# Kernel tuning notes

Hardware: AMD Instinct MI355X
Metric: run time of the kernel (lower is better)

Reference implementation:

```python
import jax, jax.numpy as jnp
import numpy as np
from jax import lax

B, T, D = 4, 4096, 1024  # d_inner == D (expansion=1.0)


def setup_inputs() -> dict:
    key = jax.random.key(0)
    ks = jax.random.split(key, 6)
    s = 1.0 / np.sqrt(D)  # xavier-ish scale
    return {
        "x": jax.random.normal(ks[0], (B, T, D), dtype=jnp.float32),
        "W_in": jax.random.normal(ks[1], (D, D), dtype=jnp.float32) * s,
        "W_alpha": jax.random.normal(ks[2], (D, D), dtype=jnp.float32) * s,
        "b_alpha": jnp.full((D,), 2.0, dtype=jnp.float32),
        "W_beta": jax.random.normal(ks[3], (D, D), dtype=jnp.float32) * s,
        "b_beta": jnp.zeros((D,), dtype=jnp.float32),
        "W_v": jax.random.normal(ks[4], (D, D), dtype=jnp.float32) * s,
        "b_v": jnp.zeros((D,), dtype=jnp.float32),
        "W_out": jax.random.normal(ks[5], (D, D), dtype=jnp.float32) * s,
    }


def reference(x, W_in, W_alpha, b_alpha, W_beta, b_beta, W_v, b_v, W_out):
    # x: [B, T, D]; torch nn.Linear convention y = x @ W.T
    xp = jax.nn.silu(jnp.einsum("btd,ed->bte", x, W_in))  # [B, T, Di]
    alpha = jax.nn.sigmoid(jnp.einsum("bte,fe->btf", xp, W_alpha) + b_alpha)
    beta = jax.nn.sigmoid(jnp.einsum("bte,fe->btf", xp, W_beta) + b_beta)
    v = jnp.tanh(jnp.einsum("bte,fe->btf", xp, W_v) + b_v)
    bv = beta * v  # precompute write term

    def step(h, ab):
        a_t, bv_t = ab  # each [B, Di]
        h = a_t * h + bv_t
        return h, h * jax.nn.silu(h)

    h0 = jnp.zeros((x.shape[0], W_alpha.shape[0]), dtype=x.dtype)
    h_last, outs = lax.scan(step, h0, (alpha.transpose(1, 0, 2), bv.transpose(1, 0, 2)))
    cell_out = outs.transpose(1, 0, 2)  # [B, T, Di]
    output = jnp.einsum("btf,df->btd", cell_out, W_out)
    return output, h_last
```

## Files before the change

### kernel.cpp

```cpp
#include <hip/hip_runtime.h>
#include <hip/hip_bf16.h>
#include <cstdint>
#include <cstddef>

typedef __bf16 bf16_t;
typedef __bf16 bf16x8 __attribute__((ext_vector_type(8)));
typedef float  f32x4  __attribute__((ext_vector_type(4)));

constexpr int kBatch = 4;
constexpr int kT = 4096;
constexpr int kD = 1024;
constexpr int kM = kBatch * kT;
constexpr int kCH = kBatch * kD;
constexpr int kNC = 128;
constexpr int kL  = kT / kNC;
constexpr int LDS_BYTES = 131072;

__device__ __forceinline__ void async16(const bf16_t* g, char* l) {
    __builtin_amdgcn_global_load_lds(
        (const __attribute__((address_space(1))) uint32_t*)g,
        (__attribute__((address_space(3))) uint32_t*)l,
        16, 0, 0);
}

__global__ void cvt_bf16_kernel(const float* __restrict__ in, bf16_t* __restrict__ out, int n8) {
    int i = blockIdx.x * blockDim.x + threadIdx.x;
    if (i >= n8) return;
    const float4* p = reinterpret_cast<const float4*>(in) + 2 * (size_t)i;
    float4 a = p[0], b = p[1];
    bf16x8 o;
    o[0] = (bf16_t)a.x; o[1] = (bf16_t)a.y; o[2] = (bf16_t)a.z; o[3] = (bf16_t)a.w;
    o[4] = (bf16_t)b.x; o[5] = (bf16_t)b.y; o[6] = (bf16_t)b.z; o[7] = (bf16_t)b.w;
    *reinterpret_cast<bf16x8*>(out + 8 * (size_t)i) = o;
}

__global__ void cvtw_kernel(const float* __restrict__ w0, const float* __restrict__ w1,
                            const float* __restrict__ w2, const float* __restrict__ w3,
                            const float* __restrict__ w4, bf16_t* __restrict__ out) {
    const int per = kD * kD / 8;
    int i = blockIdx.x * blockDim.x + threadIdx.x;
    int seg = i / per, j = i - seg * per;
    const float* src = seg == 0 ? w0 : seg == 1 ? w1 : seg == 2 ? w2 : seg == 3 ? w3 : w4;
    const float4* p = reinterpret_cast<const float4*>(src) + 2 * (size_t)j;
    float4 a = p[0], b = p[1];
    bf16x8 o;
    o[0] = (bf16_t)a.x; o[1] = (bf16_t)a.y; o[2] = (bf16_t)a.z; o[3] = (bf16_t)a.w;
    o[4] = (bf16_t)b.x; o[5] = (bf16_t)b.y; o[6] = (bf16_t)b.z; o[7] = (bf16_t)b.w;
    *reinterpret_cast<bf16x8*>(out + ((size_t)seg * per + j) * 8) = o;
}

template<int EPI>
__global__ __launch_bounds__(512, 2)
void gemm256(const bf16_t* __restrict__ A, const bf16_t* __restrict__ Bw,
             const float* __restrict__ bi0, const float* __restrict__ bi1,
             const float* __restrict__ bi2,
             void* __restrict__ out0, void* __restrict__ out1, void* __restrict__ out2,
             int M, int N, int K)
{
    extern __shared__ char lds[];
    const int tid  = threadIdx.x;
    const int lane = tid & 63;
    const int wv   = tid >> 6;
    const int wr   = wv >> 2;
    const int wc   = wv & 3;
    const int l16  = lane & 15;
    const int lhi  = lane >> 4;

    int bid = blockIdx.y * gridDim.x + blockIdx.x;
    int nwg = gridDim.x * gridDim.y;
    int swz = (bid & 7) * (nwg >> 3) + (bid >> 3);
    int gx  = N >> 8;
    int n0  = (swz % gx) << 8;
    int m0  = (swz / gx) << 8;

    auto goff = [&](int chunk) -> size_t {
        int st = chunk >> 6;
        int ri = (chunk >> 2) & 15;
        int cp = (chunk & 3) << 3;
        int cl = cp ^ (((ri >> 3) & 1) << 4);
        int gr = ((st >> 1) << 4) + ri;
        int gc = ((st & 1) << 5) + cl;
        return (size_t)gr * K + gc;
    };
    const size_t g0 = goff(tid), g1 = goff(512 + tid);
    const int d0 = wv << 10, d1 = 8192 + (wv << 10);

    auto STAGE = [&](const bf16_t* G, int row0, int k0, int lds_base) {
        const bf16_t* base = G + (size_t)row0 * K + k0;
        async16(base + g0, lds + lds_base + d0);
        async16(base + g1, lds + lds_base + d1);
    };

    auto ldsoff = [&](int r, int c) -> int {
        int ri = r & 15;
        int st = ((r >> 4) << 1) | (c >> 5);
        int cw = (c & 31) ^ (((ri >> 3) & 1) << 4);
        return (st << 10) + (ri << 6) + (cw << 1);
    };
    int offA[4][2], offB[2][2];
#pragma unroll
    for (int m = 0; m < 4; ++m)
#pragma unroll
        for (int s = 0; s < 2; ++s)
            offA[m][s] = ldsoff(wr * 64 + m * 16 + l16, s * 32 + lhi * 8);
#pragma unroll
    for (int n = 0; n < 2; ++n)
#pragma unroll
        for (int s = 0; s < 2; ++s)
            offB[n][s] = ldsoff(wc * 32 + n * 16 + l16, s * 32 + lhi * 8);

    f32x4 acc[8][4];
#pragma unroll
    for (int i = 0; i < 8; ++i)
#pragma unroll
        for (int j = 0; j < 4; ++j)
            acc[i][j] = (f32x4){0.f, 0.f, 0.f, 0.f};

    const int NT = K >> 6;

    STAGE(A,  m0,        0, 0);
    STAGE(A,  m0 + 128,  0, 16384);
    STAGE(Bw, n0,        0, 32768);
    STAGE(Bw, n0 + 128,  0, 49152);
    STAGE(A,  m0,       64, 65536);
    STAGE(Bw, n0 + 128, 64, 65536 + 49152);
    STAGE(A,  m0 + 128, 64, 65536 + 16384);
    asm volatile("s_waitcnt vmcnt(6)" ::: "memory");
    asm volatile("s_barrier" ::: "memory");

    for (int w = 0; w < NT; ++w) {
        const int bufo  = (w & 1) << 16;
        const int nbufo = bufo ^ 65536;
        const int oA0 = bufo, oA1 = bufo + 16384;
        const int oB0 = bufo + 32768, oB1 = bufo + 49152;
        const int k1 = (w + 1) << 6, k2 = (w + 2) << 6;
        bf16x8 aL[4][2], aH[4][2], bL[2][2], bH[2][2];

#pragma unroll
        for (int m = 0; m < 4; ++m)
#pragma unroll
            for (int s = 0; s < 2; ++s)
                aL[m][s] = *reinterpret_cast<const bf16x8*>(lds + oA0 + offA[m][s]);
#pragma unroll
        for (int n = 0; n < 2; ++n)
#pragma unroll
            for (int s = 0; s < 2; ++s)
                bL[n][s] = *reinterpret_cast<const bf16x8*>(lds + oB0 + offB[n][s]);
        if (w + 1 < NT) STAGE(Bw, n0, k1, nbufo + 32768);
        asm volatile("s_barrier" ::: "memory");
        __builtin_amdgcn_s_setprio(1);
#pragma unroll
        for (int m = 0; m < 4; ++m)
#pragma unroll
            for (int n = 0; n < 2; ++n)
#pragma unroll
                for (int s = 0; s < 2; ++s)
                    acc[m][n] = __builtin_amdgcn_mfma_f32_16x16x32_bf16(aL[m][s], bL[n][s], acc[m][n], 0, 0, 0);
        __builtin_amdgcn_s_setprio(0);
        asm volatile("s_barrier" ::: "memory");

#pragma unroll
        for (int n = 0; n < 2; ++n)
#pragma unroll
            for (int s = 0; s < 2; ++s)
                bH[n][s] = *reinterpret_cast<const bf16x8*>(lds + oB1 + offB[n][s]);
        if (w + 2 < NT) STAGE(A, m0, k2, oA0);
        asm volatile("s_barrier" ::: "memory");
        __builtin_amdgcn_s_setprio(1);
#pragma unroll
        for (int m = 0; m < 4; ++m)
#pragma unroll
            for (int n = 0; n < 2; ++n)
#pragma unroll
                for (int s = 0; s < 2; ++s)
                    acc[m][2 + n] = __builtin_amdgcn_mfma_f32_16x16x32_bf16(aL[m][s], bH[n][s], acc[m][2 + n], 0, 0, 0);
        __builtin_amdgcn_s_setprio(0);
        asm volatile("s_barrier" ::: "memory");

#pragma unroll
        for (int m = 0; m < 4; ++m)
#pragma unroll
            for (int s = 0; s < 2; ++s)
                aH[m][s] = *reinterpret_cast<const bf16x8*>(lds + oA1 + offA[m][s]);
        if (w + 2 < NT) STAGE(Bw, n0 + 128, k2, oB1);
        asm volatile("s_barrier" ::: "memory");
        __builtin_amdgcn_s_setprio(1);
#pragma unroll
        for (int m = 0; m < 4; ++m)
#pragma unroll
            for (int n = 0; n < 2; ++n)
#pragma unroll
                for (int s = 0; s < 2; ++s)
                    acc[4 + m][n] = __builtin_amdgcn_mfma_f32_16x16x32_bf16(aH[m][s], bL[n][s], acc[4 + m][n], 0, 0, 0);
        __builtin_amdgcn_s_setprio(0);
        asm volatile("s_barrier" ::: "memory");

        if (w + 2 < NT) STAGE(A, m0 + 128, k2, oA1);
        asm volatile("s_barrier" ::: "memory");
        __builtin_amdgcn_s_setprio(1);
#pragma unroll
        for (int m = 0; m < 4; ++m)
#pragma unroll
            for (int n = 0; n < 2; ++n)
#pragma unroll
                for (int s = 0; s < 2; ++s)
                    acc[4 + m][2 + n] = __builtin_amdgcn_mfma_f32_16x16x32_bf16(aH[m][s], bH[n][s], acc[4 + m][2 + n], 0, 0, 0);
        __builtin_amdgcn_s_setprio(0);
        if (w + 2 < NT) {
            asm volatile("s_waitcnt vmcnt(6)" ::: "memory");
        } else if (w + 2 == NT) {
            asm volatile("s_waitcnt vmcnt(0)" ::: "memory");
        }
        if (w + 1 < NT) asm volatile("s_barrier" ::: "memory");
    }

    const int slab = n0 >> 10;
    const float* bia = (EPI == 4) ? (slab == 0 ? bi0 : slab == 1 ? bi1 : bi2) : nullptr;
#pragma unroll
    for (int j = 0; j < 4; ++j) {
        const int colg = n0 + ((j >> 1) << 7) + wc * 32 + (j & 1) * 16 + l16;
        const int cL = colg & (kD - 1);
        float bs = 0.f;
        if constexpr (EPI == 4) bs = bia[cL];
#pragma unroll
        for (int i = 0; i < 8; ++i) {
            const int rb = m0 + ((i >> 2) << 7) + wr * 64 + (i & 3) * 16 + lhi * 4;
#pragma unroll
            for (int r = 0; r < 4; ++r) {
                const int rowg = rb + r;
                const float f = acc[i][j][r];
                if constexpr (EPI == 0) {
                    float s = f / (1.f + __expf(-f));
                    reinterpret_cast<bf16_t*>(out0)[(size_t)rowg * N + colg] = (bf16_t)s;
                } else if constexpr (EPI == 3) {
                    __builtin_nontemporal_store(f, reinterpret_cast<float*>(out0) + (size_t)rowg * N + colg);
                } else {
                    const size_t idx = (size_t)rowg * kD + cL;
                    if (slab == 0) {
                        float s = 1.f / (1.f + __expf(-(f + bs)));
                        __builtin_nontemporal_store(s, reinterpret_cast<float*>(out0) + idx);
                    } else if (slab == 1) {
                        float s = 1.f / (1.f + __expf(-(f + bs)));
                        __builtin_nontemporal_store((bf16_t)s, reinterpret_cast<bf16_t*>(out1) + idx);
                    } else {
                        float s = tanhf(f + bs);
                        __builtin_nontemporal_store((bf16_t)s, reinterpret_cast<bf16_t*>(out2) + idx);
                    }
                }
            }
        }
    }
}

__global__ void scan_chunk_kernel(const float* __restrict__ alpha,
                                  const bf16_t* __restrict__ beta,
                                  const bf16_t* __restrict__ vv,
                                  float* __restrict__ Aagg,
                                  float* __restrict__ Bagg)
{
    const int u  = blockIdx.x * blockDim.x + threadIdx.x;
    const int ch = u & (kCH - 1);
    const int c  = u >> 12;
    const int b  = ch >> 10;
    const int d  = ch & (kD - 1);
    size_t base = ((size_t)b * kT + (size_t)c * kL) * kD + d;
    float Ac = 1.f, Bc = 0.f;
#pragma unroll 4
    for (int t = 0; t < kL; ++t) {
        float a  = alpha[base];
        float bv = (float)beta[base] * (float)vv[base];
        Ac *= a;
        Bc = a * Bc + bv;
        base += kD;
    }
    Aagg[u] = Ac;
    Bagg[u] = Bc;
}

__global__ void scan_mid_kernel(const float* __restrict__ Aagg,
                                const float* __restrict__ Bagg,
                                float* __restrict__ Hin,
                                float* __restrict__ hlast)
{
    const int ch = blockIdx.x * blockDim.x + threadIdx.x;
    float h = 0.f;
#pragma unroll 8
    for (int c = 0; c < kNC; ++c) {
        Hin[(size_t)c * kCH + ch] = h;
        h = Aagg[(size_t)c * kCH + ch] * h + Bagg[(size_t)c * kCH + ch];
    }
    hlast[ch] = h;
}

__global__ void scan_out_kernel(const float* __restrict__ alpha,
                                const bf16_t* __restrict__ beta,
                                const bf16_t* __restrict__ vv,
                                const float* __restrict__ Hin,
                                bf16_t* __restrict__ cell)
{
    const int u  = blockIdx.x * blockDim.x + threadIdx.x;
    const int ch = u & (kCH - 1);
    const int c  = u >> 12;
    const int b  = ch >> 10;
    const int d  = ch & (kD - 1);
    size_t base = ((size_t)b * kT + (size_t)c * kL) * kD + d;
    float h = Hin[u];
#pragma unroll 4
    for (int t = 0; t < kL; ++t) {
        float a  = alpha[base];
        float bv = (float)beta[base] * (float)vv[base];
        h = a * h + bv;
        float s = 1.f / (1.f + __expf(-h));
        cell[base] = (bf16_t)(h * h * s);
        base += kD;
    }
}

extern "C" void kernel_launch(void* const* d_in, const int* in_sizes, int n_in,
                              void* d_out, int out_size, void* d_ws, size_t ws_size,
                              hipStream_t stream)
{
    const float* x     = (const float*)d_in[0];
    const float* W_in  = (const float*)d_in[1];
    const float* W_al  = (const float*)d_in[2];
    const float* b_al  = (const float*)d_in[3];
    const float* W_be  = (const float*)d_in[4];
    const float* b_be  = (const float*)d_in[5];
    const float* W_v   = (const float*)d_in[6];
    const float* b_v   = (const float*)d_in[7];
    const float* W_out = (const float*)d_in[8];

    float* out   = (float*)d_out;
    float* hlast = out + (size_t)kM * kD;

    char* ws = (char*)d_ws;
    size_t off = 0;
    auto alloc = [&](size_t bytes) -> void* {
        void* p = ws + off;
        off += (bytes + 255) & ~(size_t)255;
        return p;
    };
    bf16_t* xbf   = (bf16_t*)alloc((size_t)kM * kD * 2);
    bf16_t* xp    = (bf16_t*)alloc((size_t)kM * kD * 2);
    float*  alpha = (float*) alloc((size_t)kM * kD * 4);
    bf16_t* betab = (bf16_t*)alloc((size_t)kM * kD * 2);
    bf16_t* vb    = (bf16_t*)alloc((size_t)kM * kD * 2);
    bf16_t* wbf   = (bf16_t*)alloc((size_t)5 * kD * kD * 2);

    bf16_t* Winb = wbf;
    bf16_t* Wfus = wbf + 1 * (size_t)kD * kD;
    bf16_t* Wob  = wbf + 4 * (size_t)kD * kD;

    bf16_t* cell = xbf;
    float*  Aagg = (float*)xp;
    float*  Bagg = Aagg + (size_t)kNC * kCH;
    float*  Hin  = Bagg + (size_t)kNC * kCH;

    hipFuncSetAttribute(reinterpret_cast<const void*>(gemm256<0>), hipFuncAttributeMaxDynamicSharedMemorySize, LDS_BYTES);
    hipFuncSetAttribute(reinterpret_cast<const void*>(gemm256<3>), hipFuncAttributeMaxDynamicSharedMemorySize, LDS_BYTES);
    hipFuncSetAttribute(reinterpret_cast<const void*>(gemm256<4>), hipFuncAttributeMaxDynamicSharedMemorySize, LDS_BYTES);

    {
        int n8 = kM * kD / 8;
        cvt_bf16_kernel<<<(n8 + 255) / 256, 256, 0, stream>>>(x, xbf, n8);
        int wtot = 5 * kD * kD / 8;
        cvtw_kernel<<<(wtot + 255) / 256, 256, 0, stream>>>(W_in, W_al, W_be, W_v, W_out, wbf);
    }

    dim3 grid1(kD / 256, kM / 256);
    dim3 gridF(3 * kD / 256, kM / 256);

    gemm256<0><<<grid1, 512, LDS_BYTES, stream>>>(xbf, Winb, nullptr, nullptr, nullptr,
                                                  xp, nullptr, nullptr, kM, kD, kD);
    gemm256<4><<<gridF, 512, LDS_BYTES, stream>>>(xp, Wfus, b_al, b_be, b_v,
                                                  alpha, betab, vb, kM, 3 * kD, kD);
    scan_chunk_kernel<<<kNC * kCH / 256, 256, 0, stream>>>(alpha, betab, vb, Aagg, Bagg);
    scan_mid_kernel<<<kCH / 256, 256, 0, stream>>>(Aagg, Bagg, Hin, hlast);
    scan_out_kernel<<<kNC * kCH / 256, 256, 0, stream>>>(alpha, betab, vb, Hin, cell);

    gemm256<3><<<grid1, 512, LDS_BYTES, stream>>>(cell, Wob, nullptr, nullptr, nullptr,
                                                  out, nullptr, nullptr, kM, kD, kD);
}
```

Measured before the change: 347.2 us.

## Shrink GEMM tiles to 128x256 with K=32 steps and store alpha as fp16

The GEMM kernel is rebuilt around a 128x256 output tile with 32-wide K steps. That cuts LDS use from 128KB to 48KB and raises launch bounds to allow four blocks per CU. The staging and swizzle layout and the accumulator layout are reorganized to match. Separately, the alpha gate is written as fp16 instead of fp32, halving its write and its two reads in the scan kernels at some precision cost for the recurrence decay factor. Smaller tiles mean less data reuse per block, more blocks, and more barriers per unit of work.

```diff
diff --git a/kernel.cpp b/kernel.cpp
--- a/kernel.cpp
+++ b/kernel.cpp
@@ -4,6 +4,7 @@
 #include <cstddef>
 
 typedef __bf16 bf16_t;
+typedef _Float16 f16_t;
 typedef __bf16 bf16x8 __attribute__((ext_vector_type(8)));
 typedef float  f32x4  __attribute__((ext_vector_type(4)));
 
@@ -14,7 +15,7 @@
 constexpr int kCH = kBatch * kD;
 constexpr int kNC = 128;
 constexpr int kL  = kT / kNC;
-constexpr int LDS_BYTES = 131072;
+constexpr int LDS_BYTES = 49152;
 
 __device__ __forceinline__ void async16(const bf16_t* g, char* l) {
     __builtin_amdgcn_global_load_lds(
@@ -50,8 +51,8 @@
 }
 
 template<int EPI>
-__global__ __launch_bounds__(512, 2)
-void gemm256(const bf16_t* __restrict__ A, const bf16_t* __restrict__ Bw,
+__global__ __launch_bounds__(512, 4)
+void gemm128(const bf16_t* __restrict__ A, const bf16_t* __restrict__ Bw,
              const float* __restrict__ bi0, const float* __restrict__ bi1,
              const float* __restrict__ bi2,
              void* __restrict__ out0, void* __restrict__ out1, void* __restrict__ out2,
@@ -71,144 +72,98 @@
     int swz = (bid & 7) * (nwg >> 3) + (bid >> 3);
     int gx  = N >> 8;
     int n0  = (swz % gx) << 8;
-    int m0  = (swz / gx) << 8;
-
-    auto goff = [&](int chunk) -> size_t {
-        int st = chunk >> 6;
-        int ri = (chunk >> 2) & 15;
-        int cp = (chunk & 3) << 3;
-        int cl = cp ^ (((ri >> 3) & 1) << 4);
-        int gr = ((st >> 1) << 4) + ri;
-        int gc = ((st & 1) << 5) + cl;
-        return (size_t)gr * K + gc;
+    int m0  = (swz / gx) << 7;
+
+    const int sri = (tid >> 2) & 15;
+    const int scl = ((tid & 3) << 3) ^ ((sri & 8) << 1);
+    const int grow = ((tid >> 6) << 4) + sri;
+
+    auto STAGE = [&](const bf16_t* G, int row0, int k0, int region) {
+        async16(G + (size_t)(row0 + grow) * K + k0 + scl, lds + region + tid * 16);
     };
-    const size_t g0 = goff(tid), g1 = goff(512 + tid);
-    const int d0 = wv << 10, d1 = 8192 + (wv << 10);
-
-    auto STAGE = [&](const bf16_t* G, int row0, int k0, int lds_base) {
-        const bf16_t* base = G + (size_t)row0 * K + k0;
-        async16(base + g0, lds + lds_base + d0);
-        async16(base + g1, lds + lds_base + d1);
+
+    auto off = [&](int r, int c) -> int {
+        return ((r >> 4) << 10) + ((r & 15) << 6) + ((c ^ ((r & 8) << 1)) << 1);
     };
-
-    auto ldsoff = [&](int r, int c) -> int {
-        int ri = r & 15;
-        int st = ((r >> 4) << 1) | (c >> 5);
-        int cw = (c & 31) ^ (((ri >> 3) & 1) << 4);
-        return (st << 10) + (ri << 6) + (cw << 1);
-    };
-    int offA[4][2], offB[2][2];
+    int offA[4], offB[4];
 #pragma unroll
     for (int m = 0; m < 4; ++m)
-#pragma unroll
-        for (int s = 0; s < 2; ++s)
-            offA[m][s] = ldsoff(wr * 64 + m * 16 + l16, s * 32 + lhi * 8);
-#pragma unroll
-    for (int n = 0; n < 2; ++n)
-#pragma unroll
-        for (int s = 0; s < 2; ++s)
-            offB[n][s] = ldsoff(wc * 32 + n * 16 + l16, s * 32 + lhi * 8);
-
-    f32x4 acc[8][4];
-#pragma unroll
-    for (int i = 0; i < 8; ++i)
+        offA[m] = off(wr * 64 + m * 16 + l16, lhi * 8);
+#pragma unroll
+    for (int n = 0; n < 4; ++n)
+        offB[n] = 8192 + (n >> 1) * 8192 + off(wc * 32 + (n & 1) * 16 + l16, lhi * 8);
+
+    f32x4 acc[4][4];
+#pragma unroll
+    for (int i = 0; i < 4; ++i)
 #pragma unroll
         for (int j = 0; j < 4; ++j)
             acc[i][j] = (f32x4){0.f, 0.f, 0.f, 0.f};
 
-    const int NT = K >> 6;
-
-    STAGE(A,  m0,        0, 0);
-    STAGE(A,  m0 + 128,  0, 16384);
-    STAGE(Bw, n0,        0, 32768);
-    STAGE(Bw, n0 + 128,  0, 49152);
-    STAGE(A,  m0,       64, 65536);
-    STAGE(Bw, n0 + 128, 64, 65536 + 49152);
-    STAGE(A,  m0 + 128, 64, 65536 + 16384);
-    asm volatile("s_waitcnt vmcnt(6)" ::: "memory");
+    const int NT = K >> 5;
+
+    STAGE(A,  m0,       0, 0);
+    STAGE(Bw, n0,       0, 8192);
+    STAGE(Bw, n0 + 128, 0, 16384);
+    STAGE(A,  m0,       32, 24576);
+    STAGE(Bw, n0,       32, 24576 + 8192);
+    STAGE(Bw, n0 + 128, 32, 24576 + 16384);
+    asm volatile("s_waitcnt vmcnt(3)" ::: "memory");
     asm volatile("s_barrier" ::: "memory");
 
     for (int w = 0; w < NT; ++w) {
-        const int bufo  = (w & 1) << 16;
-        const int nbufo = bufo ^ 65536;
-        const int oA0 = bufo, oA1 = bufo + 16384;
-        const int oB0 = bufo + 32768, oB1 = bufo + 49152;
-        const int k1 = (w + 1) << 6, k2 = (w + 2) << 6;
-        bf16x8 aL[4][2], aH[4][2], bL[2][2], bH[2][2];
-
-#pragma unroll
-        for (int m = 0; m < 4; ++m)
-#pragma unroll
-            for (int s = 0; s < 2; ++s)
-                aL[m][s] = *reinterpret_cast<const bf16x8*>(lds + oA0 + offA[m][s]);
-#pragma unroll
-        for (int n = 0; n < 2; ++n)
-#pragma unroll
-            for (int s = 0; s < 2; ++s)
-                bL[n][s] = *reinterpret_cast<const bf16x8*>(lds + oB0 + offB[n][s]);
-        if (w + 1 < NT) STAGE(Bw, n0, k1, nbufo + 32768);
+        const int bufo = (w & 1) * 24576;
+        const int k2   = (w + 2) << 5;
+        bf16x8 aLo[2], aHi[2], bLo[2], bHi[2];
+
+        aLo[0] = *reinterpret_cast<const bf16x8*>(lds + bufo + offA[0]);
+        aLo[1] = *reinterpret_cast<const bf16x8*>(lds + bufo + offA[1]);
+        bLo[0] = *reinterpret_cast<const bf16x8*>(lds + bufo + offB[0]);
+        bLo[1] = *reinterpret_cast<const bf16x8*>(lds + bufo + offB[1]);
         asm volatile("s_barrier" ::: "memory");
         __builtin_amdgcn_s_setprio(1);
-#pragma unroll
-        for (int m = 0; m < 4; ++m)
-#pragma unroll
-            for (int n = 0; n < 2; ++n)
-#pragma unroll
-                for (int s = 0; s < 2; ++s)
-                    acc[m][n] = __builtin_amdgcn_mfma_f32_16x16x32_bf16(aL[m][s], bL[n][s], acc[m][n], 0, 0, 0);
+        acc[0][0] = __builtin_amdgcn_mfma_f32_16x16x32_bf16(aLo[0], bLo[0], acc[0][0], 0, 0, 0);
+        acc[0][1] = __builtin_amdgcn_mfma_f32_16x16x32_bf16(aLo[0], bLo[1], acc[0][1], 0, 0, 0);
+        acc[1][0] = __builtin_amdgcn_mfma_f32_16x16x32_bf16(aLo[1], bLo[0], acc[1][0], 0, 0, 0);
+        acc[1][1] = __builtin_amdgcn_mfma_f32_16x16x32_bf16(aLo[1], bLo[1], acc[1][1], 0, 0, 0);
         __builtin_amdgcn_s_setprio(0);
         asm volatile("s_barrier" ::: "memory");
 
-#pragma unroll
-        for (int n = 0; n < 2; ++n)
-#pragma unroll
-            for (int s = 0; s < 2; ++s)
-                bH[n][s] = *reinterpret_cast<const bf16x8*>(lds + oB1 + offB[n][s]);
-        if (w + 2 < NT) STAGE(A, m0, k2, oA0);
+        bHi[0] = *reinterpret_cast<const bf16x8*>(lds + bufo + offB[2]);
+        bHi[1] = *reinterpret_cast<const bf16x8*>(lds + bufo + offB[3]);
+        if (w + 2 < NT) STAGE(Bw, n0, k2, bufo + 8192);
         asm volatile("s_barrier" ::: "memory");
         __builtin_amdgcn_s_setprio(1);
-#pragma unroll
-        for (int m = 0; m < 4; ++m)
-#pragma unroll
-            for (int n = 0; n < 2; ++n)
-#pragma unroll
-                for (int s = 0; s < 2; ++s)
-                    acc[m][2 + n] = __builtin_amdgcn_mfma_f32_16x16x32_bf16(aL[m][s], bH[n][s], acc[m][2 + n], 0, 0, 0);
+        acc[0][2] = __builtin_amdgcn_mfma_f32_16x16x32_bf16(aLo[0], bHi[0], acc[0][2], 0, 0, 0);
+        acc[0][3] = __builtin_amdgcn_mfma_f32_16x16x32_bf16(aLo[0], bHi[1], acc[0][3], 0, 0, 0);
+        acc[1][2] = __builtin_amdgcn_mfma_f32_16x16x32_bf16(aLo[1], bHi[0], acc[1][2], 0, 0, 0);
+        acc[1][3] = __builtin_amdgcn_mfma_f32_16x16x32_bf16(aLo[1], bHi[1], acc[1][3], 0, 0, 0);
         __builtin_amdgcn_s_setprio(0);
         asm volatile("s_barrier" ::: "memory");
 
-#pragma unroll
-        for (int m = 0; m < 4; ++m)
-#pragma unroll
-            for (int s = 0; s < 2; ++s)
-                aH[m][s] = *reinterpret_cast<const bf16x8*>(lds + oA1 + offA[m][s]);
-        if (w + 2 < NT) STAGE(Bw, n0 + 128, k2, oB1);
+        aHi[0] = *reinterpret_cast<const bf16x8*>(lds + bufo + offA[2]);
+        aHi[1] = *reinterpret_cast<const bf16x8*>(lds + bufo + offA[3]);
+        if (w + 2 < NT) STAGE(Bw, n0 + 128, k2, bufo + 16384);
         asm volatile("s_barrier" ::: "memory");
         __builtin_amdgcn_s_setprio(1);
-#pragma unroll
-        for (int m = 0; m < 4; ++m)
-#pragma unroll
-            for (int n = 0; n < 2; ++n)
-#pragma unroll
-                for (int s = 0; s < 2; ++s)
-                    acc[4 + m][n] = __builtin_amdgcn_mfma_f32_16x16x32_bf16(aH[m][s], bL[n][s], acc[4 + m][n], 0, 0, 0);
+        acc[2][0] = __builtin_amdgcn_mfma_f32_16x16x32_bf16(aHi[0], bLo[0], acc[2][0], 0, 0, 0);
+        acc[2][1] = __builtin_amdgcn_mfma_f32_16x16x32_bf16(aHi[0], bLo[1], acc[2][1], 0, 0, 0);
+        acc[3][0] = __builtin_amdgcn_mfma_f32_16x16x32_bf16(aHi[1], bLo[0], acc[3][0], 0, 0, 0);
+        acc[3][1] = __builtin_amdgcn_mfma_f32_16x16x32_bf16(aHi[1], bLo[1], acc[3][1], 0, 0, 0);
         __builtin_amdgcn_s_setprio(0);
         asm volatile("s_barrier" ::: "memory");
 
-        if (w + 2 < NT) STAGE(A, m0 + 128, k2, oA1);
+        if (w + 2 < NT) STAGE(A, m0, k2, bufo);
         asm volatile("s_barrier" ::: "memory");
         __builtin_amdgcn_s_setprio(1);
-#pragma unroll
-        for (int m = 0; m < 4; ++m)
-#pragma unroll
-            for (int n = 0; n < 2; ++n)
-#pragma unroll
-                for (int s = 0; s < 2; ++s)
-                    acc[4 + m][2 + n] = __builtin_amdgcn_mfma_f32_16x16x32_bf16(aH[m][s], bH[n][s], acc[4 + m][2 + n], 0, 0, 0);
+        acc[2][2] = __builtin_amdgcn_mfma_f32_16x16x32_bf16(aHi[0], bHi[0], acc[2][2], 0, 0, 0);
+        acc[2][3] = __builtin_amdgcn_mfma_f32_16x16x32_bf16(aHi[0], bHi[1], acc[2][3], 0, 0, 0);
+        acc[3][2] = __builtin_amdgcn_mfma_f32_16x16x32_bf16(aHi[1], bHi[0], acc[3][2], 0, 0, 0);
+        acc[3][3] = __builtin_amdgcn_mfma_f32_16x16x32_bf16(aHi[1], bHi[1], acc[3][3], 0, 0, 0);
         __builtin_amdgcn_s_setprio(0);
         if (w + 2 < NT) {
-            asm volatile("s_waitcnt vmcnt(6)" ::: "memory");
-        } else if (w + 2 == NT) {
+            asm volatile("s_waitcnt vmcnt(3)" ::: "memory");
+        } else if (w + 1 < NT) {
             asm volatile("s_waitcnt vmcnt(0)" ::: "memory");
         }
         if (w + 1 < NT) asm volatile("s_barrier" ::: "memory");
@@ -223,8 +178,8 @@
         float bs = 0.f;
         if constexpr (EPI == 4) bs = bia[cL];
 #pragma unroll
-        for (int i = 0; i < 8; ++i) {
-            const int rb = m0 + ((i >> 2) << 7) + wr * 64 + (i & 3) * 16 + lhi * 4;
+        for (int i = 0; i < 4; ++i) {
+            const int rb = m0 + wr * 64 + i * 16 + lhi * 4;
 #pragma unroll
             for (int r = 0; r < 4; ++r) {
                 const int rowg = rb + r;
@@ -238,7 +193,7 @@
                     const size_t idx = (size_t)rowg * kD + cL;
                     if (slab == 0) {
                         float s = 1.f / (1.f + __expf(-(f + bs)));
-                        __builtin_nontemporal_store(s, reinterpret_cast<float*>(out0) + idx);
+                        __builtin_nontemporal_store((f16_t)s, reinterpret_cast<f16_t*>(out0) + idx);
                     } else if (slab == 1) {
                         float s = 1.f / (1.f + __expf(-(f + bs)));
                         __builtin_nontemporal_store((bf16_t)s, reinterpret_cast<bf16_t*>(out1) + idx);
@@ -252,7 +207,7 @@
     }
 }
 
-__global__ void scan_chunk_kernel(const float* __restrict__ alpha,
+__global__ void scan_chunk_kernel(const f16_t* __restrict__ alpha,
                                   const bf16_t* __restrict__ beta,
                                   const bf16_t* __restrict__ vv,
                                   float* __restrict__ Aagg,
@@ -267,7 +222,7 @@
     float Ac = 1.f, Bc = 0.f;
 #pragma unroll 4
     for (int t = 0; t < kL; ++t) {
-        float a  = alpha[base];
+        float a  = (float)alpha[base];
         float bv = (float)beta[base] * (float)vv[base];
         Ac *= a;
         Bc = a * Bc + bv;
@@ -292,7 +247,7 @@
     hlast[ch] = h;
 }
 
-__global__ void scan_out_kernel(const float* __restrict__ alpha,
+__global__ void scan_out_kernel(const f16_t* __restrict__ alpha,
                                 const bf16_t* __restrict__ beta,
                                 const bf16_t* __restrict__ vv,
                                 const float* __restrict__ Hin,
@@ -307,7 +262,7 @@
     float h = Hin[u];
 #pragma unroll 4
     for (int t = 0; t < kL; ++t) {
-        float a  = alpha[base];
+        float a  = (float)alpha[base];
         float bv = (float)beta[base] * (float)vv[base];
         h = a * h + bv;
         float s = 1.f / (1.f + __expf(-h));
@@ -342,7 +297,7 @@
     };
     bf16_t* xbf   = (bf16_t*)alloc((size_t)kM * kD * 2);
     bf16_t* xp    = (bf16_t*)alloc((size_t)kM * kD * 2);
-    float*  alpha = (float*) alloc((size_t)kM * kD * 4);
+    f16_t*  alpha = (f16_t*) alloc((size_t)kM * kD * 2);
     bf16_t* betab = (bf16_t*)alloc((size_t)kM * kD * 2);
     bf16_t* vb    = (bf16_t*)alloc((size_t)kM * kD * 2);
     bf16_t* wbf   = (bf16_t*)alloc((size_t)5 * kD * kD * 2);
@@ -356,9 +311,9 @@
     float*  Bagg = Aagg + (size_t)kNC * kCH;
     float*  Hin  = Bagg + (size_t)kNC * kCH;
 
-    hipFuncSetAttribute(reinterpret_cast<const void*>(gemm256<0>), hipFuncAttributeMaxDynamicSharedMemorySize, LDS_BYTES);
-    hipFuncSetAttribute(reinterpret_cast<const void*>(gemm256<3>), hipFuncAttributeMaxDynamicSharedMemorySize, LDS_BYTES);
-    hipFuncSetAttribute(reinterpret_cast<const void*>(gemm256<4>), hipFuncAttributeMaxDynamicSharedMemorySize, LDS_BYTES);
+    hipFuncSetAttribute(reinterpret_cast<const void*>(gemm128<0>), hipFuncAttributeMaxDynamicSharedMemorySize, LDS_BYTES);
+    hipFuncSetAttribute(reinterpret_cast<const void*>(gemm128<3>), hipFuncAttributeMaxDynamicSharedMemorySize, LDS_BYTES);
+    hipFuncSetAttribute(reinterpret_cast<const void*>(gemm128<4>), hipFuncAttributeMaxDynamicSharedMemorySize, LDS_BYTES);
 
     {
         int n8 = kM * kD / 8;
@@ -367,17 +322,17 @@
         cvtw_kernel<<<(wtot + 255) / 256, 256, 0, stream>>>(W_in, W_al, W_be, W_v, W_out, wbf);
     }
 
-    dim3 grid1(kD / 256, kM / 256);
-    dim3 gridF(3 * kD / 256, kM / 256);
-
-    gemm256<0><<<grid1, 512, LDS_BYTES, stream>>>(xbf, Winb, nullptr, nullptr, nullptr,
+    dim3 grid1(kD / 256, kM / 128);
+    dim3 gridF(3 * kD / 256, kM / 128);
+
+    gemm128<0><<<grid1, 512, LDS_BYTES, stream>>>(xbf, Winb, nullptr, nullptr, nullptr,
                                                   xp, nullptr, nullptr, kM, kD, kD);
-    gemm256<4><<<gridF, 512, LDS_BYTES, stream>>>(xp, Wfus, b_al, b_be, b_v,
+    gemm128<4><<<gridF, 512, LDS_BYTES, stream>>>(xp, Wfus, b_al, b_be, b_v,
                                                   alpha, betab, vb, kM, 3 * kD, kD);
     scan_chunk_kernel<<<kNC * kCH / 256, 256, 0, stream>>>(alpha, betab, vb, Aagg, Bagg);
     scan_mid_kernel<<<kCH / 256, 256, 0, stream>>>(Aagg, Bagg, Hin, hlast);
     scan_out_kernel<<<kNC * kCH / 256, 256, 0, stream>>>(alpha, betab, vb, Hin, cell);
 
-    gemm256<3><<<grid1, 512, LDS_BYTES, stream>>>(cell, Wob, nullptr, nullptr, nullptr,
+    gemm128<3><<<grid1, 512, LDS_BYTES, stream>>>(cell, Wob, nullptr, nullptr, nullptr,
                                                   out, nullptr, nullptr, kM, kD, kD);
 }
```

Result: no change. 346.6 us (-0.2%).

## Simplify GEMM main loop to whole-tile prefetch and store alpha as fp16

Applied to the files above, without the earlier changes.

Replaces the fine-grained four-phase GEMM pipeline, which staged sub-tiles two steps ahead behind many barriers, with a simple double buffer. The whole next K-tile is prefetched at the start of each iteration, and one wait plus one barrier follows the MFMA work. Separately, the sigmoid alpha gate is stored as fp16 instead of fp32, halving its write and its reads in both scan kernels. The simpler pipeline overlaps less finely and waits on vmcnt(0) every tile. fp16 alpha costs precision in a long multiplicative recurrence.

```diff
diff --git a/kernel.cpp b/kernel.cpp
--- a/kernel.cpp
+++ b/kernel.cpp
@@ -4,6 +4,7 @@
 #include <cstddef>
 
 typedef __bf16 bf16_t;
+typedef _Float16 f16_t;
 typedef __bf16 bf16x8 __attribute__((ext_vector_type(8)));
 typedef float  f32x4  __attribute__((ext_vector_type(4)));
 
@@ -90,6 +91,13 @@
         async16(base + g0, lds + lds_base + d0);
         async16(base + g1, lds + lds_base + d1);
     };
+    auto STAGE_TILE = [&](int w, int bufo) {
+        const int k0 = w << 6;
+        STAGE(A,  m0,        k0, bufo);
+        STAGE(A,  m0 + 128,  k0, bufo + 16384);
+        STAGE(Bw, n0,        k0, bufo + 32768);
+        STAGE(Bw, n0 + 128,  k0, bufo + 49152);
+    };
 
     auto ldsoff = [&](int r, int c) -> int {
         int ri = r & 15;
@@ -118,14 +126,8 @@
 
     const int NT = K >> 6;
 
-    STAGE(A,  m0,        0, 0);
-    STAGE(A,  m0 + 128,  0, 16384);
-    STAGE(Bw, n0,        0, 32768);
-    STAGE(Bw, n0 + 128,  0, 49152);
-    STAGE(A,  m0,       64, 65536);
-    STAGE(Bw, n0 + 128, 64, 65536 + 49152);
-    STAGE(A,  m0 + 128, 64, 65536 + 16384);
-    asm volatile("s_waitcnt vmcnt(6)" ::: "memory");
+    STAGE_TILE(0, 0);
+    asm volatile("s_waitcnt vmcnt(0)" ::: "memory");
     asm volatile("s_barrier" ::: "memory");
 
     for (int w = 0; w < NT; ++w) {
@@ -133,85 +135,47 @@
         const int nbufo = bufo ^ 65536;
         const int oA0 = bufo, oA1 = bufo + 16384;
         const int oB0 = bufo + 32768, oB1 = bufo + 49152;
-        const int k1 = (w + 1) << 6, k2 = (w + 2) << 6;
-        bf16x8 aL[4][2], aH[4][2], bL[2][2], bH[2][2];
-
-#pragma unroll
-        for (int m = 0; m < 4; ++m)
-#pragma unroll
-            for (int s = 0; s < 2; ++s)
-                aL[m][s] = *reinterpret_cast<const bf16x8*>(lds + oA0 + offA[m][s]);
-#pragma unroll
-        for (int n = 0; n < 2; ++n)
-#pragma unroll
-            for (int s = 0; s < 2; ++s)
-                bL[n][s] = *reinterpret_cast<const bf16x8*>(lds + oB0 + offB[n][s]);
-        if (w + 1 < NT) STAGE(Bw, n0, k1, nbufo + 32768);
-        asm volatile("s_barrier" ::: "memory");
-        __builtin_amdgcn_s_setprio(1);
-#pragma unroll
-        for (int m = 0; m < 4; ++m)
-#pragma unroll
-            for (int n = 0; n < 2; ++n)
-#pragma unroll
-                for (int s = 0; s < 2; ++s)
-                    acc[m][n] = __builtin_amdgcn_mfma_f32_16x16x32_bf16(aL[m][s], bL[n][s], acc[m][n], 0, 0, 0);
-        __builtin_amdgcn_s_setprio(0);
-        asm volatile("s_barrier" ::: "memory");
-
-#pragma unroll
-        for (int n = 0; n < 2; ++n)
-#pragma unroll
-            for (int s = 0; s < 2; ++s)
-                bH[n][s] = *reinterpret_cast<const bf16x8*>(lds + oB1 + offB[n][s]);
-        if (w + 2 < NT) STAGE(A, m0, k2, oA0);
-        asm volatile("s_barrier" ::: "memory");
-        __builtin_amdgcn_s_setprio(1);
-#pragma unroll
-        for (int m = 0; m < 4; ++m)
-#pragma unroll
-            for (int n = 0; n < 2; ++n)
-#pragma unroll
-                for (int s = 0; s < 2; ++s)
-                    acc[m][2 + n] = __builtin_amdgcn_mfma_f32_16x16x32_bf16(aL[m][s], bH[n][s], acc[m][2 + n], 0, 0, 0);
-        __builtin_amdgcn_s_setprio(0);
-        asm volatile("s_barrier" ::: "memory");
-
-#pragma unroll
-        for (int m = 0; m < 4; ++m)
-#pragma unroll
-            for (int s = 0; s < 2; ++s)
-                aH[m][s] = *reinterpret_cast<const bf16x8*>(lds + oA1 + offA[m][s]);
-        if (w + 2 < NT) STAGE(Bw, n0 + 128, k2, oB1);
-        asm volatile("s_barrier" ::: "memory");
-        __builtin_amdgcn_s_setprio(1);
-#pragma unroll
-        for (int m = 0; m < 4; ++m)
-#pragma unroll
-            for (int n = 0; n < 2; ++n)
-#pragma unroll
-                for (int s = 0; s < 2; ++s)
-                    acc[4 + m][n] = __builtin_amdgcn_mfma_f32_16x16x32_bf16(aH[m][s], bL[n][s], acc[4 + m][n], 0, 0, 0);
-        __builtin_amdgcn_s_setprio(0);
-        asm volatile("s_barrier" ::: "memory");
-
-        if (w + 2 < NT) STAGE(A, m0 + 128, k2, oA1);
-        asm volatile("s_barrier" ::: "memory");
-        __builtin_amdgcn_s_setprio(1);
-#pragma unroll
-        for (int m = 0; m < 4; ++m)
-#pragma unroll
-            for (int n = 0; n < 2; ++n)
-#pragma unroll
-                for (int s = 0; s < 2; ++s)
-                    acc[4 + m][2 + n] = __builtin_amdgcn_mfma_f32_16x16x32_bf16(aH[m][s], bH[n][s], acc[4 + m][2 + n], 0, 0, 0);
-        __builtin_amdgcn_s_setprio(0);
-        if (w + 2 < NT) {
-            asm volatile("s_waitcnt vmcnt(6)" ::: "memory");
-        } else if (w + 2 == NT) {
+
+        if (w + 1 < NT) STAGE_TILE(w + 1, nbufo);
+
+#pragma unroll
+        for (int s = 0; s < 2; ++s) {
+            bf16x8 aL[4], aH[4], bL[2], bH[2];
+#pragma unroll
+            for (int m = 0; m < 4; ++m)
+                aL[m] = *reinterpret_cast<const bf16x8*>(lds + oA0 + offA[m][s]);
+#pragma unroll
+            for (int n = 0; n < 2; ++n) {
+                bL[n] = *reinterpret_cast<const bf16x8*>(lds + oB0 + offB[n][s]);
+                bH[n] = *reinterpret_cast<const bf16x8*>(lds + oB1 + offB[n][s]);
+            }
+            __builtin_amdgcn_s_setprio(1);
+#pragma unroll
+            for (int m = 0; m < 4; ++m)
+#pragma unroll
+                for (int n = 0; n < 2; ++n) {
+                    acc[m][n]     = __builtin_amdgcn_mfma_f32_16x16x32_bf16(aL[m], bL[n], acc[m][n], 0, 0, 0);
+                    acc[m][2 + n] = __builtin_amdgcn_mfma_f32_16x16x32_bf16(aL[m], bH[n], acc[m][2 + n], 0, 0, 0);
+                }
+            __builtin_amdgcn_s_setprio(0);
+#pragma unroll
+            for (int m = 0; m < 4; ++m)
+                aH[m] = *reinterpret_cast<const bf16x8*>(lds + oA1 + offA[m][s]);
+            __builtin_amdgcn_s_setprio(1);
+#pragma unroll
+            for (int m = 0; m < 4; ++m)
+#pragma unroll
+                for (int n = 0; n < 2; ++n) {
+                    acc[4 + m][n]     = __builtin_amdgcn_mfma_f32_16x16x32_bf16(aH[m], bL[n], acc[4 + m][n], 0, 0, 0);
+                    acc[4 + m][2 + n] = __builtin_amdgcn_mfma_f32_16x16x32_bf16(aH[m], bH[n], acc[4 + m][2 + n], 0, 0, 0);
+                }
+            __builtin_amdgcn_s_setprio(0);
+        }
+
+        if (w + 1 < NT) {
             asm volatile("s_waitcnt vmcnt(0)" ::: "memory");
+            asm volatile("s_barrier" ::: "memory");
         }
-        if (w + 1 < NT) asm volatile("s_barrier" ::: "memory");
     }
 
     const int slab = n0 >> 10;
@@ -238,7 +202,7 @@
                     const size_t idx = (size_t)rowg * kD + cL;
                     if (slab == 0) {
                         float s = 1.f / (1.f + __expf(-(f + bs)));
-                        __builtin_nontemporal_store(s, reinterpret_cast<float*>(out0) + idx);
+                        __builtin_nontemporal_store((f16_t)s, reinterpret_cast<f16_t*>(out0) + idx);
                     } else if (slab == 1) {
                         float s = 1.f / (1.f + __expf(-(f + bs)));
                         __builtin_nontemporal_store((bf16_t)s, reinterpret_cast<bf16_t*>(out1) + idx);
@@ -252,7 +216,7 @@
     }
 }
 
-__global__ void scan_chunk_kernel(const float* __restrict__ alpha,
+__global__ void scan_chunk_kernel(const f16_t* __restrict__ alpha,
                                   const bf16_t* __restrict__ beta,
                                   const bf16_t* __restrict__ vv,
                                   float* __restrict__ Aagg,
@@ -267,7 +231,7 @@
     float Ac = 1.f, Bc = 0.f;
 #pragma unroll 4
     for (int t = 0; t < kL; ++t) {
-        float a  = alpha[base];
+        float a  = (float)alpha[base];
         float bv = (float)beta[base] * (float)vv[base];
         Ac *= a;
         Bc = a * Bc + bv;
@@ -292,7 +256,7 @@
     hlast[ch] = h;
 }
 
-__global__ void scan_out_kernel(const float* __restrict__ alpha,
+__global__ void scan_out_kernel(const f16_t* __restrict__ alpha,
                                 const bf16_t* __restrict__ beta,
                                 const bf16_t* __restrict__ vv,
                                 const float* __restrict__ Hin,
@@ -307,7 +271,7 @@
     float h = Hin[u];
 #pragma unroll 4
     for (int t = 0; t < kL; ++t) {
-        float a  = alpha[base];
+        float a  = (float)alpha[base];
         float bv = (float)beta[base] * (float)vv[base];
         h = a * h + bv;
         float s = 1.f / (1.f + __expf(-h));
@@ -342,7 +306,7 @@
     };
     bf16_t* xbf   = (bf16_t*)alloc((size_t)kM * kD * 2);
     bf16_t* xp    = (bf16_t*)alloc((size_t)kM * kD * 2);
-    float*  alpha = (float*) alloc((size_t)kM * kD * 4);
+    f16_t*  alpha = (f16_t*) alloc((size_t)kM * kD * 2);
     bf16_t* betab = (bf16_t*)alloc((size_t)kM * kD * 2);
     bf16_t* vb    = (bf16_t*)alloc((size_t)kM * kD * 2);
     bf16_t* wbf   = (bf16_t*)alloc((size_t)5 * kD * kD * 2);
```

Measured after the change: 342.1 us. About the same (-1.5%).
